# Performance work log

Hardware: AMD Instinct MI355X
Metric: run time of the kernel (lower is better)

## Reference

```python
import jax, jax.numpy as jnp
import numpy as np

D_MODEL = 1024
DK = 64
H = D_MODEL // DK
EPS = 1e-5


def setup_inputs() -> dict:
    key = jax.random.key(0)
    ks = jax.random.split(key, 8)
    B, M = 4, 2048
    s = 1.0 / np.sqrt(D_MODEL)
    return {
        "inp": jax.random.normal(ks[0], (B, M, D_MODEL), dtype=jnp.float32),
        "Wq": jax.random.normal(ks[1], (D_MODEL, D_MODEL), dtype=jnp.float32) * s,
        "bq": jnp.zeros((D_MODEL,), dtype=jnp.float32),
        "Wk": jax.random.normal(ks[2], (D_MODEL, D_MODEL), dtype=jnp.float32) * s,
        "bk": jnp.zeros((D_MODEL,), dtype=jnp.float32),
        "Wv": jax.random.normal(ks[3], (D_MODEL, D_MODEL), dtype=jnp.float32) * s,
        "bv": jnp.zeros((D_MODEL,), dtype=jnp.float32),
        "gamma": jnp.ones((D_MODEL,), dtype=jnp.float32),
        "beta": jnp.zeros((D_MODEL,), dtype=jnp.float32),
    }


def reference(inp, Wq, bq, Wk, bk, Wv, bv, gamma, beta):
    B, M, _ = inp.shape
    # LayerNorm over last dim
    mu = jnp.mean(inp, axis=-1, keepdims=True)
    var = jnp.mean(jnp.square(inp - mu), axis=-1, keepdims=True)
    out = (inp - mu) * jax.lax.rsqrt(var + EPS) * gamma + beta
    # QKV projections (x @ W + b)
    Q = (out @ Wq + bq).reshape(B, M, DK, H)
    K = (out @ Wk + bk).reshape(B, M, DK, H)
    V = (out @ Wv + bv).reshape(B, M, DK, H)
    # per-position attention over the dk axis, contracting h
    scores = jnp.einsum("bmih,bmjh->bmij", Q, K) / np.sqrt(DK)  # [B,M,dk,dk]
    att = jax.nn.softmax(scores, axis=-1)
    res = jnp.einsum("bmij,bmjh->bmih", att, V).reshape(B, M, D_MODEL)
    # dropout is identity at eval; positionals add in original is dead code
    return inp + res
```

## Files before the change

kernel.cpp:

```cpp
#include <hip/hip_runtime.h>
#include <hip/hip_bf16.h>

#define D_MODEL 1024
#define NQKV 3072

typedef __attribute__((ext_vector_type(8))) short bf16x8;
typedef __attribute__((ext_vector_type(4))) float f32x4;
typedef __attribute__((ext_vector_type(16))) float f32x16;
typedef __attribute__((ext_vector_type(8))) unsigned short u16x8;

static __device__ __forceinline__ unsigned short f2bf(float f){
  unsigned int x = __float_as_uint(f);
  x += 0x7fff + ((x >> 16) & 1);
  return (unsigned short)(x >> 16);
}
static __device__ __forceinline__ float bf2f(unsigned short u){
  return __uint_as_float(((unsigned int)u) << 16);
}

__global__ __launch_bounds__(256) void ln_kernel(const float* __restrict__ inp,
    const float* __restrict__ gamma, const float* __restrict__ beta,
    unsigned short* __restrict__ X){
  const int row = blockIdx.x;
  const int t = threadIdx.x;
  const float4* ip = (const float4*)(inp + (size_t)row * D_MODEL);
  float4 v = ip[t];
  float s1 = v.x + v.y + v.z + v.w;
  float s2 = v.x*v.x + v.y*v.y + v.z*v.z + v.w*v.w;
#pragma unroll
  for (int off = 32; off >= 1; off >>= 1){
    s1 += __shfl_down(s1, off);
    s2 += __shfl_down(s2, off);
  }
  __shared__ float red[8];
  const int wave = t >> 6, lane = t & 63;
  if (lane == 0){ red[wave] = s1; red[4 + wave] = s2; }
  __syncthreads();
  s1 = red[0] + red[1] + red[2] + red[3];
  s2 = red[4] + red[5] + red[6] + red[7];
  const float mu   = s1 * (1.0f / D_MODEL);
  const float var  = s2 * (1.0f / D_MODEL) - mu * mu;
  const float rstd = rsqrtf(var + 1e-5f);
  float4 g = ((const float4*)gamma)[t];
  float4 b = ((const float4*)beta)[t];
  ushort4 o;
  o.x = f2bf((v.x - mu) * rstd * g.x + b.x);
  o.y = f2bf((v.y - mu) * rstd * g.y + b.y);
  o.z = f2bf((v.z - mu) * rstd * g.z + b.z);
  o.w = f2bf((v.w - mu) * rstd * g.w + b.w);
  ((ushort4*)(X + (size_t)row * D_MODEL))[t] = o;
}

__global__ __launch_bounds__(256) void wtrans_kernel(const float* __restrict__ Wq,
    const float* __restrict__ Wk, const float* __restrict__ Wv,
    unsigned short* __restrict__ Wt){
  __shared__ float tile[32][33];
  const float* W = (blockIdx.z == 0) ? Wq : ((blockIdx.z == 1) ? Wk : Wv);
  const int k0 = blockIdx.x * 32, n0 = blockIdx.y * 32;
  const int r = threadIdx.x >> 5, c = threadIdx.x & 31;
#pragma unroll
  for (int i = 0; i < 4; i++)
    tile[r + i*8][c] = W[(size_t)(k0 + r + i*8) * D_MODEL + n0 + c];
  __syncthreads();
  unsigned short* dst = Wt + (size_t)(blockIdx.z * D_MODEL + n0) * D_MODEL + k0;
#pragma unroll
  for (int i = 0; i < 4; i++){
    int rr = r + i*8;
    dst[(size_t)rr * D_MODEL + c] = f2bf(tile[c][rr]);
  }
}

__global__ void biascat_kernel(const float* __restrict__ bq, const float* __restrict__ bk,
                               const float* __restrict__ bv, float* __restrict__ bc){
  int i = blockIdx.x * 256 + threadIdx.x;
  float v = (i < 1024) ? bq[i] : (i < 2048) ? bk[i - 1024] : bv[i - 2048];
  bc[i] = v;
}


#define GLL(src, dst) __builtin_amdgcn_global_load_lds( \
    (const __attribute__((address_space(1))) void*)(src), \
    (__attribute__((address_space(3))) void*)(dst), 16, 0, 0)

#define STAGE(tsrc, bi) do { \
  _Pragma("unroll") \
  for (int q = 0; q < 4; q++){ \
    const int idx = q*256 + tid; \
    const int row = idx >> 3; \
    const size_t scol = (size_t)((tsrc)*128) + (((idx & 7)*16) ^ ((row & 7) << 4)); \
    GLL(Ag + (size_t)row*2048 + scol, ldsS + (size_t)(bi)*32768 + idx*16); \
    GLL(Bg + (size_t)row*2048 + scol, ldsS + (size_t)(bi)*32768 + 16384 + idx*16); \
  } \
} while(0)

#define BODY(bi) do { \
  const char* Ab = ldsS + (size_t)(bi)*32768 + (wm*64 + lr)*128; \
  const char* Bb = ldsS + (size_t)(bi)*32768 + 16384 + (wn*64 + lr)*128; \
  bf16x8 Ar[4][2], Br[4][2]; \
  _Pragma("unroll") \
  for (int m = 0; m < 4; m++){ \
    Ar[m][0] = *(const bf16x8*)(Ab + m*2048 + colb0); \
    Ar[m][1] = *(const bf16x8*)(Ab + m*2048 + colb1); \
  } \
  _Pragma("unroll") \
  for (int n = 0; n < 4; n++){ \
    Br[n][0] = *(const bf16x8*)(Bb + n*2048 + colb0); \
    Br[n][1] = *(const bf16x8*)(Bb + n*2048 + colb1); \
  } \
  _Pragma("unroll") \
  for (int m = 0; m < 4; m++) \
    _Pragma("unroll") \
    for (int n = 0; n < 4; n++){ \
      acc[m][n] = __builtin_amdgcn_mfma_f32_16x16x32_bf16(Ar[m][0], Br[n][0], acc[m][n], 0, 0, 0); \
      acc[m][n] = __builtin_amdgcn_mfma_f32_16x16x32_bf16(Ar[m][1], Br[n][1], acc[m][n], 0, 0, 0); \
    } \
} while(0)

#define BARRIER __builtin_amdgcn_s_barrier()
#define SCHEDB  __builtin_amdgcn_sched_barrier(0)
#define VMCNT0  asm volatile("s_waitcnt vmcnt(0)" ::: "memory")

__global__ __launch_bounds__(256, 2) void gemm128_kernel(const unsigned short* __restrict__ A,
    const unsigned short* __restrict__ Bt, const float* __restrict__ bias,
    unsigned short* __restrict__ C){
  __shared__ __align__(16) char ldsS[2 * 32768];
  const int tid = threadIdx.x;
  const int wave = tid >> 6, lane = tid & 63;
  const int wm = wave >> 1, wn = wave & 1;
  const int lr = lane & 15;
  const int x7 = (lane & 7) << 4;
  const int colb0 = ((lane >> 4) * 16) ^ x7;
  const int colb1 = (64 + (lane >> 4) * 16) ^ x7;

  const int b = blockIdx.x;
  const int swz = (b & 7) * 192 + (b >> 3);
  const int m0 = (swz & 63) * 128;
  const int n0 = (swz >> 6) * 128;

  const char* Ag = (const char*)(A + (size_t)m0 * 1024);
  const char* Bg = (const char*)(Bt + (size_t)n0 * 1024);

  f32x4 acc[4][4] = {};

  STAGE(0, 0);

  int buf = 0;
  for (int t = 0; t < 16; ++t, buf ^= 1){
    SCHEDB; VMCNT0; BARRIER; SCHEDB;
    if (t < 15) STAGE(t + 1, buf ^ 1);
    BODY(buf);
  }

  const int gm = m0 + wm*64;
  const int gn = n0 + wn*64;
  const int rr0 = (lane >> 4) * 4;
#pragma unroll
  for (int nf = 0; nf < 4; nf++){
    const int gcol = gn + nf*16 + lr;
    const float bb = bias[gcol];
#pragma unroll
    for (int mf = 0; mf < 4; mf++){
      const int grow = gm + mf*16 + rr0;
#pragma unroll
      for (int r = 0; r < 4; r++)
        C[(size_t)(grow + r) * NQKV + gcol] = f2bf(acc[mf][nf][r] + bb);
    }
  }
}

__global__ __launch_bounds__(256) void attn_kernel(const unsigned short* __restrict__ qkv,
    const float* __restrict__ inp, float* __restrict__ out){
  __shared__ unsigned short P[4][64 * 64];
  const int wave = threadIdx.x >> 6, lane = threadIdx.x & 63;
  const int token = blockIdx.x * 4 + wave;
  const unsigned short* row = qkv + (size_t)token * NQKV;
  const int l31 = lane & 31, hi = lane >> 5;
  const int l15 = lane & 15, qg = lane >> 4;
  char* pbase = (char*)&P[wave][0];

  bf16x8 kf[2], qf[2];
#pragma unroll
  for (int mt = 0; mt < 2; mt++)
    kf[mt] = *(const bf16x8*)(row + 1024 + (mt*32 + l31)*16 + hi*8);
#pragma unroll
  for (int nt = 0; nt < 2; nt++)
    qf[nt] = *(const bf16x8*)(row + (nt*32 + l31)*16 + hi*8);

  bf16x8 vf[2];
#pragma unroll
  for (int kc = 0; kc < 2; kc++)
#pragma unroll
    for (int e = 0; e < 8; e++)
      vf[kc][e] = (short)row[2048 + (kc*32 + qg*8 + e)*16 + l15];

  f32x16 s[2][2] = {};
#pragma unroll
  for (int mt = 0; mt < 2; mt++)
#pragma unroll
    for (int nt = 0; nt < 2; nt++)
      s[mt][nt] = __builtin_amdgcn_mfma_f32_32x32x16_bf16(kf[mt], qf[nt], s[mt][nt], 0, 0, 0);

#pragma unroll
  for (int ti = 0; ti < 2; ti++){
    float m = s[0][ti][0];
#pragma unroll
    for (int mt = 0; mt < 2; mt++)
#pragma unroll
      for (int r = 0; r < 16; r++) m = fmaxf(m, s[mt][ti][r]);
    m = fmaxf(m, __shfl_xor(m, 32));
    float sum = 0.0f;
#pragma unroll
    for (int mt = 0; mt < 2; mt++)
#pragma unroll
      for (int r = 0; r < 16; r++){
        float p = exp2f((s[mt][ti][r] - m) * 0.1803368801f);
        s[mt][ti][r] = p;
        sum += p;
      }
    sum += __shfl_xor(sum, 32);
    const float invs = 1.0f / sum;
    const int i = ti*32 + l31;
    const int sw = (i & 7) << 4;
#pragma unroll
    for (int mt = 0; mt < 2; mt++)
#pragma unroll
      for (int g = 0; g < 4; g++){
        ushort4 pk;
        pk.x = f2bf(s[mt][ti][4*g + 0] * invs);
        pk.y = f2bf(s[mt][ti][4*g + 1] * invs);
        pk.z = f2bf(s[mt][ti][4*g + 2] * invs);
        pk.w = f2bf(s[mt][ti][4*g + 3] * invs);
        const int jbyte = mt*64 + g*16 + hi*8;
        *(ushort4*)(pbase + ((i*128 + jbyte) ^ sw)) = pk;
      }
  }
  __syncthreads();

  f32x4 o[4] = {};
#pragma unroll
  for (int nt = 0; nt < 4; nt++){
    const int n = nt*16 + l15;
    const int swr = (n & 7) << 4;
#pragma unroll
    for (int kc = 0; kc < 2; kc++){
      bf16x8 pb = *(const bf16x8*)(pbase + ((n*128 + kc*64 + qg*16) ^ swr));
      o[nt] = __builtin_amdgcn_mfma_f32_16x16x32_bf16(vf[kc], pb, o[nt], 0, 0, 0);
    }
  }

  const size_t base = (size_t)token * D_MODEL;
#pragma unroll
  for (int nt = 0; nt < 4; nt++){
    const int i = nt*16 + l15;
    const float4 iv = *(const float4*)(inp + base + i*16 + qg*4);
    float4 ov;
    ov.x = iv.x + o[nt][0];
    ov.y = iv.y + o[nt][1];
    ov.z = iv.z + o[nt][2];
    ov.w = iv.w + o[nt][3];
    *(float4*)(out + base + i*16 + qg*4) = ov;
  }
}

extern "C" void kernel_launch(void* const* d_in, const int* in_sizes, int n_in,
                              void* d_out, int out_size, void* d_ws, size_t ws_size,
                              hipStream_t stream) {
  const float* inp   = (const float*)d_in[0];
  const float* Wq    = (const float*)d_in[1];
  const float* bq    = (const float*)d_in[2];
  const float* Wk    = (const float*)d_in[3];
  const float* bk    = (const float*)d_in[4];
  const float* Wv    = (const float*)d_in[5];
  const float* bv    = (const float*)d_in[6];
  const float* gamma = (const float*)d_in[7];
  const float* beta  = (const float*)d_in[8];
  float* out = (float*)d_out;

  char* ws = (char*)d_ws;
  unsigned short* Xln  = (unsigned short*)ws;
  unsigned short* Wt   = (unsigned short*)(ws + 16777216);
  float*          bc   = (float*)(ws + 23068672);
  unsigned short* QKV  = (unsigned short*)(ws + 23080960);

  ln_kernel<<<8192, 256, 0, stream>>>(inp, gamma, beta, Xln);
  wtrans_kernel<<<dim3(32, 32, 3), 256, 0, stream>>>(Wq, Wk, Wv, Wt);
  biascat_kernel<<<12, 256, 0, stream>>>(bq, bk, bv, bc);
  gemm128_kernel<<<1536, 256, 0, stream>>>(Xln, Wt, bc, QKV);
  attn_kernel<<<2048, 256, 0, stream>>>(QKV, inp, out);
}
```

Baseline: 109.3 us.

## Enlarge QKV GEMM tile to 256x256 with 8 waves per block

Changes the projection GEMM from 128x128 tiles with 4 waves to 256x256 tiles with 8 waves. Each wave now computes a 128x64 sub-tile, and the grid shrinks from 1536 to 384 blocks. The goal is higher arithmetic intensity per LDS byte and fewer global reloads of the A and B panels. The cost is 128KB of LDS per block for double buffering and higher accumulator register pressure. With only 384 blocks, occupancy may be limited to one block per CU and the last wave of blocks may leave CUs idle.

```diff
diff --git a/kernel.cpp b/kernel.cpp
--- a/kernel.cpp
+++ b/kernel.cpp
@@ -85,62 +85,58 @@
 #define STAGE(tsrc, bi) do { \
   _Pragma("unroll") \
   for (int q = 0; q < 4; q++){ \
-    const int idx = q*256 + tid; \
+    const int idx = q*512 + tid; \
     const int row = idx >> 3; \
     const size_t scol = (size_t)((tsrc)*128) + (((idx & 7)*16) ^ ((row & 7) << 4)); \
-    GLL(Ag + (size_t)row*2048 + scol, ldsS + (size_t)(bi)*32768 + idx*16); \
-    GLL(Bg + (size_t)row*2048 + scol, ldsS + (size_t)(bi)*32768 + 16384 + idx*16); \
+    GLL(Ag + (size_t)row*2048 + scol, ldsS + (size_t)(bi)*65536 + idx*16); \
+    GLL(Bg + (size_t)row*2048 + scol, ldsS + (size_t)(bi)*65536 + 32768 + idx*16); \
   } \
 } while(0)
 
 #define BODY(bi) do { \
-  const char* Ab = ldsS + (size_t)(bi)*32768 + (wm*64 + lr)*128; \
-  const char* Bb = ldsS + (size_t)(bi)*32768 + 16384 + (wn*64 + lr)*128; \
-  bf16x8 Ar[4][2], Br[4][2]; \
+  const char* Ab = ldsS + (size_t)(bi)*65536 + (wr*128 + lr)*128; \
+  const char* Bb = ldsS + (size_t)(bi)*65536 + 32768 + (wc*64 + lr)*128; \
   _Pragma("unroll") \
-  for (int m = 0; m < 4; m++){ \
-    Ar[m][0] = *(const bf16x8*)(Ab + m*2048 + colb0); \
-    Ar[m][1] = *(const bf16x8*)(Ab + m*2048 + colb1); \
+  for (int kh = 0; kh < 2; kh++){ \
+    const int cb = kh ? colb1 : colb0; \
+    bf16x8 Ar[8], Br[4]; \
+    _Pragma("unroll") \
+    for (int m = 0; m < 8; m++) Ar[m] = *(const bf16x8*)(Ab + m*2048 + cb); \
+    _Pragma("unroll") \
+    for (int n = 0; n < 4; n++) Br[n] = *(const bf16x8*)(Bb + n*2048 + cb); \
+    _Pragma("unroll") \
+    for (int m = 0; m < 8; m++) \
+      _Pragma("unroll") \
+      for (int n = 0; n < 4; n++) \
+        acc[m][n] = __builtin_amdgcn_mfma_f32_16x16x32_bf16(Ar[m], Br[n], acc[m][n], 0, 0, 0); \
   } \
-  _Pragma("unroll") \
-  for (int n = 0; n < 4; n++){ \
-    Br[n][0] = *(const bf16x8*)(Bb + n*2048 + colb0); \
-    Br[n][1] = *(const bf16x8*)(Bb + n*2048 + colb1); \
-  } \
-  _Pragma("unroll") \
-  for (int m = 0; m < 4; m++) \
-    _Pragma("unroll") \
-    for (int n = 0; n < 4; n++){ \
-      acc[m][n] = __builtin_amdgcn_mfma_f32_16x16x32_bf16(Ar[m][0], Br[n][0], acc[m][n], 0, 0, 0); \
-      acc[m][n] = __builtin_amdgcn_mfma_f32_16x16x32_bf16(Ar[m][1], Br[n][1], acc[m][n], 0, 0, 0); \
-    } \
 } while(0)
 
 #define BARRIER __builtin_amdgcn_s_barrier()
 #define SCHEDB  __builtin_amdgcn_sched_barrier(0)
 #define VMCNT0  asm volatile("s_waitcnt vmcnt(0)" ::: "memory")
 
-__global__ __launch_bounds__(256, 2) void gemm128_kernel(const unsigned short* __restrict__ A,
+__global__ __launch_bounds__(512, 2) void gemm256_kernel(const unsigned short* __restrict__ A,
     const unsigned short* __restrict__ Bt, const float* __restrict__ bias,
     unsigned short* __restrict__ C){
-  __shared__ __align__(16) char ldsS[2 * 32768];
+  __shared__ __align__(16) char ldsS[2 * 65536];
   const int tid = threadIdx.x;
   const int wave = tid >> 6, lane = tid & 63;
-  const int wm = wave >> 1, wn = wave & 1;
+  const int wr = wave >> 2, wc = wave & 3;
   const int lr = lane & 15;
   const int x7 = (lane & 7) << 4;
   const int colb0 = ((lane >> 4) * 16) ^ x7;
   const int colb1 = (64 + (lane >> 4) * 16) ^ x7;
 
   const int b = blockIdx.x;
-  const int swz = (b & 7) * 192 + (b >> 3);
-  const int m0 = (swz & 63) * 128;
-  const int n0 = (swz >> 6) * 128;
+  const int swz = (b & 7) * 48 + (b >> 3);
+  const int m0 = (swz & 31) * 256;
+  const int n0 = (swz >> 5) * 256;
 
   const char* Ag = (const char*)(A + (size_t)m0 * 1024);
   const char* Bg = (const char*)(Bt + (size_t)n0 * 1024);
 
-  f32x4 acc[4][4] = {};
+  f32x4 acc[8][4] = {};
 
   STAGE(0, 0);
 
@@ -151,15 +147,15 @@
     BODY(buf);
   }
 
-  const int gm = m0 + wm*64;
-  const int gn = n0 + wn*64;
+  const int gm = m0 + wr*128;
+  const int gn = n0 + wc*64;
   const int rr0 = (lane >> 4) * 4;
 #pragma unroll
   for (int nf = 0; nf < 4; nf++){
     const int gcol = gn + nf*16 + lr;
     const float bb = bias[gcol];
 #pragma unroll
-    for (int mf = 0; mf < 4; mf++){
+    for (int mf = 0; mf < 8; mf++){
       const int grow = gm + mf*16 + rr0;
 #pragma unroll
       for (int r = 0; r < 4; r++)
@@ -285,6 +281,6 @@
   ln_kernel<<<8192, 256, 0, stream>>>(inp, gamma, beta, Xln);
   wtrans_kernel<<<dim3(32, 32, 3), 256, 0, stream>>>(Wq, Wk, Wv, Wt);
   biascat_kernel<<<12, 256, 0, stream>>>(bq, bk, bv, bc);
-  gemm128_kernel<<<1536, 256, 0, stream>>>(Xln, Wt, bc, QKV);
+  gemm256_kernel<<<384, 512, 0, stream>>>(Xln, Wt, bc, QKV);
   attn_kernel<<<2048, 256, 0, stream>>>(QKV, inp, out);
 }
```

Result: faster. 105.2 us (-3.8%).
